# Kernel optimization log

Measured on AMD Instinct MI355X. Metric: run time of the kernel, lower is better.

The kernel has to match this reference:

```python
import jax, jax.numpy as jnp
import numpy as np

B, S, D, H, F = 2, 2048, 1024, 16, 64  # batch, seq, d_model, heads, head_dim


def setup_inputs() -> dict:
    key = jax.random.key(0)
    ks = jax.random.split(key, 7)
    return {
        "q": jax.random.normal(ks[0], (B, S, D), dtype=jnp.float32),
        "k": jax.random.normal(ks[1], (B, S, D), dtype=jnp.float32),
        "v": jax.random.normal(ks[2], (B, S, D), dtype=jnp.float32),
        "Wq": jax.random.normal(ks[3], (H, D, F), dtype=jnp.float32) * 0.02,
        "Wk": jax.random.normal(ks[4], (H, D, F), dtype=jnp.float32) * 0.02,
        "Wv": jax.random.normal(ks[5], (H, D, F), dtype=jnp.float32) * 0.02,
        "Wo": jax.random.normal(ks[6], (H * F, D), dtype=jnp.float32) * 0.02,
    }


def reference(q, k, v, Wq, Wk, Wv, Wo):
    head_dim = Wq.shape[-1]
    queries = jnp.einsum('bqo,hof->bhqf', q, Wq)
    keys = jnp.einsum('bko,hof->bhkf', k, Wk)
    values = jnp.einsum('bvo,hof->bhvf', v, Wv)
    # K.batch_dot(queries, keys, axes=[3,3]) -> [b,h,q,k]
    scores = jnp.einsum('bhqf,bhkf->bhqk', queries, keys) / jnp.sqrt(
        jnp.asarray(head_dim, dtype=queries.dtype))
    attn = jax.nn.softmax(scores, axis=-1)
    # Faithful to K.batch_dot(attn, values, axes=[2,2]):
    # contracts the QUERY axis of attn with the seq axis of values -> A^T V
    out4 = jnp.einsum('bhqk,bhqf->bhkf', attn, values)  # [b,h,s,f]
    b = out4.shape[0]
    # Faithful raw reshape [b,h,s,f] -> [b,s,h*f] (no transpose, as in original)
    out = out4.reshape(b, out4.shape[2], -1)
    return out @ Wo  # [b,s,d_model]
```

## Files before the change

kernel.cpp:

```cpp
#include <hip/hip_runtime.h>
#include <hip/hip_bf16.h>
#include <stdint.h>

#define Bc 2
#define Sc 2048
#define Dc 1024
#define Hc 16
#define Fc 64
constexpr int BHSF = Bc * Hc * Sc * Fc;

typedef __attribute__((ext_vector_type(8))) short bf16x8;
typedef __attribute__((ext_vector_type(4))) short bf16x4;
typedef __attribute__((ext_vector_type(4))) float f32x4;

#define MFMA16(a, b, c) __builtin_amdgcn_mfma_f32_16x16x32_bf16(a, b, c, 0, 0, 0)
#define EXP2(x) __builtin_amdgcn_exp2f(x)
#define SCALE2 0.18033688f

__device__ inline short f2bfn(float x) {
    __hip_bfloat16 h = __float2bfloat16(x);
    return __builtin_bit_cast(short, h);
}
__device__ inline uint32_t cvt2(float lo, float hi) {
    uint32_t a = (uint16_t)f2bfn(lo);
    uint32_t b = (uint16_t)f2bfn(hi);
    return a | (b << 16);
}
__device__ inline float bf2f(short s) {
    uint32_t u = ((uint32_t)(uint16_t)s) << 16;
    return __builtin_bit_cast(float, u);
}

__global__ __launch_bounds__(256) void tcvt_all_kernel(
    const float* __restrict__ Wq, const float* __restrict__ Wk,
    const float* __restrict__ Wv, const float* __restrict__ Wo,
    short* __restrict__ WqT, short* __restrict__ WkT,
    short* __restrict__ WvT, short* __restrict__ WoT)
{
    __shared__ short td[64 * 72];
    const int t = threadIdx.x;
    const int sr = t >> 2, sc = (t & 3) * 16;
    const int zp = blockIdx.z;
    const int m0 = blockIdx.x * 64;

    const float* in; short* out; int N, n0;
    if (zp < 48) {
        const int sel = zp >> 4, h = zp & 15;
        in  = ((sel == 0) ? Wq : (sel == 1) ? Wk : Wv) + (size_t)h * Dc * Fc;
        out = ((sel == 0) ? WqT : (sel == 1) ? WkT : WvT) + (size_t)h * Fc * Dc;
        N = Fc; n0 = 0;
    } else {
        in = Wo; out = WoT; N = Dc; n0 = (zp - 48) * 64;
    }

    const float* src = in + (size_t)(m0 + sr) * N + n0 + sc;
    #pragma unroll
    for (int i = 0; i < 16; i += 4) {
        f32x4 a = *(const f32x4*)(src + i);
        td[sr * 72 + sc + i + 0] = f2bfn(a[0]);
        td[sr * 72 + sc + i + 1] = f2bfn(a[1]);
        td[sr * 72 + sc + i + 2] = f2bfn(a[2]);
        td[sr * 72 + sc + i + 3] = f2bfn(a[3]);
    }
    __syncthreads();
    alignas(16) short vals[16];
    #pragma unroll
    for (int i = 0; i < 16; ++i) vals[i] = td[(sc + i) * 72 + sr];
    short* dst = out + (size_t)(n0 + sr) * Dc + m0 + sc;
    *(bf16x8*)dst       = *(const bf16x8*)&vals[0];
    *(bf16x8*)(dst + 8) = *(const bf16x8*)&vals[8];
}

__global__ __launch_bounds__(256) void proj_kernel(
    const float* __restrict__ xq, const float* __restrict__ xk,
    const float* __restrict__ xv,
    const short* __restrict__ WqT, const short* __restrict__ WkT,
    const short* __restrict__ WvT,
    short* __restrict__ Qo, short* __restrict__ Ko, short* __restrict__ VtO)
{
    const int mt = blockIdx.x, hp = blockIdx.y, z = blockIdx.z;
    const float* x  = (z == 0) ? xq : (z == 1) ? xk : xv;
    const short* Wt = ((z == 0) ? WqT : (z == 1) ? WkT : WvT) + (size_t)hp * 128 * Dc;
    const int m0 = mt * 128;

    __shared__ short xs[2][128 * 40];
    __shared__ short ws[2][128 * 40];

    const int t = threadIdx.x, lane = t & 63, w = t >> 6;
    const int wm = w >> 1, wn = w & 1;
    const int l15 = lane & 15, g = lane >> 4;
    const int str = t >> 1, stc = (t & 1) * 16;

    f32x4 xg[4]; bf16x8 wg[2];
    auto gload = [&](int d0) {
        const float* s = &x[(size_t)(m0 + str) * Dc + d0 + stc];
        #pragma unroll
        for (int j = 0; j < 4; ++j) xg[j] = ((const f32x4*)s)[j];
        const short* ww = &Wt[(size_t)str * Dc + d0 + stc];
        wg[0] = *(const bf16x8*)ww;
        wg[1] = *(const bf16x8*)(ww + 8);
    };
    auto swrite = [&](int buf) {
        bf16x8 p0, p1;
        #pragma unroll
        for (int i = 0; i < 4; ++i) {
            p0[i] = f2bfn(xg[0][i]); p0[4 + i] = f2bfn(xg[1][i]);
            p1[i] = f2bfn(xg[2][i]); p1[4 + i] = f2bfn(xg[3][i]);
        }
        *(bf16x8*)&xs[buf][str * 40 + stc]     = p0;
        *(bf16x8*)&xs[buf][str * 40 + stc + 8] = p1;
        *(bf16x8*)&ws[buf][str * 40 + stc]     = wg[0];
        *(bf16x8*)&ws[buf][str * 40 + stc + 8] = wg[1];
    };

    f32x4 acc[4][4];
    #pragma unroll
    for (int i = 0; i < 4; ++i)
        #pragma unroll
        for (int j = 0; j < 4; ++j) acc[i][j] = (f32x4){0.f, 0.f, 0.f, 0.f};

    gload(0); swrite(0); gload(32);

    auto step = [&](int d0, int cur) {
        __syncthreads();
        if (d0 + 32 < Dc) swrite(cur ^ 1);
        if (d0 + 64 < Dc) gload(d0 + 64);
        bf16x8 afr[4], bfr[4];
        #pragma unroll
        for (int ms = 0; ms < 4; ++ms)
            afr[ms] = *(const bf16x8*)&xs[cur][(wm * 64 + ms * 16 + l15) * 40 + g * 8];
        #pragma unroll
        for (int fb = 0; fb < 4; ++fb)
            bfr[fb] = *(const bf16x8*)&ws[cur][(wn * 64 + fb * 16 + l15) * 40 + g * 8];
        #pragma unroll
        for (int ms = 0; ms < 4; ++ms)
            #pragma unroll
            for (int fb = 0; fb < 4; ++fb)
                acc[ms][fb] = MFMA16(afr[ms], bfr[fb], acc[ms][fb]);
    };

    for (int d0 = 0; d0 < Dc; d0 += 64) {
        step(d0, 0);
        step(d0 + 32, 1);
    }

    const float oscale = (z == 0) ? SCALE2 : 1.0f;
    __syncthreads();
    {
        short* bb = wn ? &ws[0][0] : &xs[0][0];
        #pragma unroll
        for (int ms = 0; ms < 4; ++ms)
            #pragma unroll
            for (int fb = 0; fb < 4; ++fb)
                #pragma unroll
                for (int r = 0; r < 4; ++r)
                    bb[(wm * 64 + ms * 16 + g * 4 + r) * 80 + fb * 16 + l15] =
                        f2bfn(acc[ms][fb][r] * oscale);
    }
    __syncthreads();

    const int b = m0 >> 11, s0 = m0 & 2047;
    if (z < 2) {
        const int row = t & 127, half = t >> 7;
        const short* src = (half ? &ws[0][0] : &xs[0][0]) + row * 80;
        short* outp = ((z == 0) ? Qo : Ko)
                    + ((size_t)(b * Hc + hp * 2 + half) * Sc + s0 + row) * Fc;
        #pragma unroll
        for (int j = 0; j < 64; j += 8)
            *(bf16x8*)&outp[j] = *(const bf16x8*)&src[j];
    } else {
        const int fhr = t & 127, half = fhr >> 6, f = fhr & 63;
        const int colg = t >> 7;
        const short* src = half ? &ws[0][0] : &xs[0][0];
        short* o = VtO + ((size_t)(b * Hc + hp * 2 + half) * Fc + f) * Sc
                       + s0 + colg * 64;
        alignas(16) short vals[64];
        #pragma unroll
        for (int j = 0; j < 64; ++j) vals[j] = src[(colg * 64 + j) * 80 + f];
        #pragma unroll
        for (int j = 0; j < 64; j += 8)
            *(bf16x8*)(o + j) = *(const bf16x8*)&vals[j];
    }
}

__global__ __launch_bounds__(256) void stats_kernel(
    const short* __restrict__ Qg, const short* __restrict__ Kg,
    float* __restrict__ mrow)
{
    const int q0 = blockIdx.x * 128;
    const int bh = blockIdx.y;
    const short* Qb = Qg + (size_t)bh * Sc * Fc;
    const short* Kb = Kg + (size_t)bh * Sc * Fc;

    __shared__ short ksA[64 * 72], ksB[64 * 72];

    const int t = threadIdx.x, lane = t & 63, w = t >> 6;
    const int l15 = lane & 15, g = lane >> 4;
    const int sr4 = t >> 2, sc4 = (t & 3) * 16;

    bf16x8 qf[2][2];
    #pragma unroll
    for (int qs2 = 0; qs2 < 2; ++qs2)
        #pragma unroll
        for (int kc2 = 0; kc2 < 2; ++kc2)
            qf[qs2][kc2] = *(const bf16x8*)
                &Qb[(size_t)(q0 + w * 32 + qs2 * 16 + l15) * Fc + kc2 * 32 + g * 8];

    bf16x8 kr0, kr1;
    auto gload = [&](int kt) {
        const short* s = &Kb[(size_t)(kt + sr4) * Fc + sc4];
        kr0 = *(const bf16x8*)s;
        kr1 = *(const bf16x8*)(s + 8);
    };
    auto swrite = [&](short* d) {
        *(bf16x8*)&d[sr4 * 72 + sc4]     = kr0;
        *(bf16x8*)&d[sr4 * 72 + sc4 + 8] = kr1;
    };

    f32x4 ls[2];
    ls[0] = (f32x4){0.f, 0.f, 0.f, 0.f};
    ls[1] = (f32x4){0.f, 0.f, 0.f, 0.f};

    gload(0); swrite(ksA); gload(64);

    auto half = [&](int kt, const short* cur, short* nxt) {
        __syncthreads();
        if (kt + 64 < Sc) swrite(nxt);
        if (kt + 128 < Sc) gload(kt + 128);
        #pragma unroll
        for (int kf = 0; kf < 4; ++kf) {
            bf16x8 a0 = *(const bf16x8*)&cur[(kf * 16 + l15) * 72 + 0  + g * 8];
            bf16x8 a1 = *(const bf16x8*)&cur[(kf * 16 + l15) * 72 + 32 + g * 8];
            #pragma unroll
            for (int qs2 = 0; qs2 < 2; ++qs2) {
                f32x4 acc = (f32x4){0.f, 0.f, 0.f, 0.f};
                acc = MFMA16(a0, qf[qs2][0], acc);
                acc = MFMA16(a1, qf[qs2][1], acc);
                #pragma unroll
                for (int r = 0; r < 4; ++r) ls[qs2][r] += EXP2(acc[r]);
            }
        }
    };

    for (int kt = 0; kt < Sc; kt += 128) {
        half(kt,      ksA, ksB);
        half(kt + 64, ksB, ksA);
    }

    #pragma unroll
    for (int qs2 = 0; qs2 < 2; ++qs2) {
        float l = (ls[qs2][0] + ls[qs2][1]) + (ls[qs2][2] + ls[qs2][3]);
        l += __shfl_xor(l, 16, 64);
        l += __shfl_xor(l, 32, 64);
        if (lane < 16)
            mrow[bh * Sc + q0 + w * 32 + qs2 * 16 + l15] = __log2f(l);
    }
}

__global__ __launch_bounds__(256) void attn_kernel(
    const short* __restrict__ Qg, const short* __restrict__ Kg,
    const short* __restrict__ VtG, const float* __restrict__ mrow,
    short* __restrict__ O4a, short* __restrict__ O4b)
{
    const int k0 = blockIdx.x * 256;
    const int qh = blockIdx.y;
    const int bh = blockIdx.z;
    const int qbeg = qh * 1024, qend = qbeg + 1024;
    const short* Qb = Qg  + (size_t)bh * Sc * Fc;
    const short* Kb = Kg  + (size_t)bh * Sc * Fc;
    const short* Vb = VtG + (size_t)bh * Fc * Sc;
    const float* mb = mrow + (size_t)bh * Sc;

    __shared__ short qs[64 * 72];
    __shared__ short vt[64 * 72];
    __shared__ short pl[256 * 72];

    const int t = threadIdx.x, lane = t & 63, w = t >> 6;
    const int l15 = lane & 15, g = lane >> 4;
    const int sr8 = t >> 2, sc8 = (t & 3) * 16;

    bf16x8 kf[4][2];
    #pragma unroll
    for (int ks = 0; ks < 4; ++ks)
        #pragma unroll
        for (int kc = 0; kc < 2; ++kc)
            kf[ks][kc] = *(const bf16x8*)
                &Kb[(size_t)(k0 + w * 64 + ks * 16 + l15) * Fc + kc * 32 + g * 8];

    f32x4 oacc[4][4];
    #pragma unroll
    for (int i = 0; i < 4; ++i)
        #pragma unroll
        for (int j = 0; j < 4; ++j) oacc[i][j] = (f32x4){0.f, 0.f, 0.f, 0.f};

    bf16x8 qr0, qr1, vr0, vr1;
    auto gload = [&](int qn) {
        const short* s = &Qb[(size_t)(qn + sr8) * Fc + sc8];
        qr0 = *(const bf16x8*)s;
        qr1 = *(const bf16x8*)(s + 8);
        const short* v = &Vb[(size_t)sr8 * Sc + qn + sc8];
        vr0 = *(const bf16x8*)v;
        vr1 = *(const bf16x8*)(v + 8);
    };

    gload(qbeg);

    for (int q0 = qbeg; q0 < qend; q0 += 64) {
        __syncthreads();
        *(bf16x8*)&qs[sr8 * 72 + sc8]     = qr0;
        *(bf16x8*)&qs[sr8 * 72 + sc8 + 8] = qr1;
        *(bf16x8*)&vt[sr8 * 72 + sc8]     = vr0;
        *(bf16x8*)&vt[sr8 * 72 + sc8 + 8] = vr1;
        if (q0 + 64 < qend) gload(q0 + 64);
        f32x4 mq[4];
        #pragma unroll
        for (int qf = 0; qf < 4; ++qf)
            mq[qf] = *(const f32x4*)&mb[q0 + qf * 16 + g * 4];
        __syncthreads();

        #pragma unroll
        for (int qf = 0; qf < 4; ++qf) {
            bf16x8 qa0 = *(const bf16x8*)&qs[(qf * 16 + l15) * 72 + 0  + g * 8];
            bf16x8 qa1 = *(const bf16x8*)&qs[(qf * 16 + l15) * 72 + 32 + g * 8];
            #pragma unroll
            for (int ks = 0; ks < 4; ++ks) {
                f32x4 acc = (f32x4){0.f, 0.f, 0.f, 0.f};
                acc = MFMA16(qa0, kf[ks][0], acc);
                acc = MFMA16(qa1, kf[ks][1], acc);
                uint2 pv;
                pv.x = cvt2(EXP2(acc[0] - mq[qf][0]), EXP2(acc[1] - mq[qf][1]));
                pv.y = cvt2(EXP2(acc[2] - mq[qf][2]), EXP2(acc[3] - mq[qf][3]));
                *(uint2*)&pl[(w * 64 + ks * 16 + l15) * 72 + qf * 16 + g * 4] = pv;
            }
        }
        __syncthreads();

        #pragma unroll
        for (int qc = 0; qc < 64; qc += 32) {
            bf16x8 pa[4], vbf[4];
            #pragma unroll
            for (int ks = 0; ks < 4; ++ks)
                pa[ks] = *(const bf16x8*)&pl[(w * 64 + ks * 16 + l15) * 72 + qc + g * 8];
            #pragma unroll
            for (int fb = 0; fb < 4; ++fb)
                vbf[fb] = *(const bf16x8*)&vt[(fb * 16 + l15) * 72 + qc + g * 8];
            #pragma unroll
            for (int ks = 0; ks < 4; ++ks)
                #pragma unroll
                for (int fb = 0; fb < 4; ++fb)
                    oacc[ks][fb] = MFMA16(pa[ks], vbf[fb], oacc[ks][fb]);
        }
    }

    __syncthreads();
    #pragma unroll
    for (int ks = 0; ks < 4; ++ks)
        #pragma unroll
        for (int fb = 0; fb < 4; ++fb)
            #pragma unroll
            for (int r = 0; r < 4; ++r)
                pl[(w * 64 + ks * 16 + g * 4 + r) * 72 + fb * 16 + l15] =
                    f2bfn(oacc[ks][fb][r]);
    __syncthreads();
    {
        short* O = qh ? O4b : O4a;
        short* o = O + ((size_t)bh * Sc + k0 + t) * Fc;
        #pragma unroll
        for (int j = 0; j < 64; j += 8)
            *(bf16x8*)&o[j] = *(const bf16x8*)&pl[t * 72 + j];
    }
}

__global__ __launch_bounds__(256) void outgemm_kernel(
    const short* __restrict__ Aa, const short* __restrict__ Ab,
    const short* __restrict__ WoT, float* __restrict__ out)
{
    const int m0 = blockIdx.x * 128, n0 = blockIdx.y * 64;

    __shared__ short asA[128 * 72], asB[128 * 72];
    __shared__ short wsA[64 * 72],  wsB[64 * 72];

    const int t = threadIdx.x, lane = t & 63, w = t >> 6;
    const int l15 = lane & 15, g = lane >> 4;
    const int ar = t >> 1, ac = (t & 1) * 32;
    const int wr = t >> 2, wc = (t & 3) * 16;

    bf16x8 ag0[4], ag1[4], wg[2];
    auto gload = [&](int d0) {
        const short* s0 = &Aa[(size_t)(m0 + ar) * Dc + d0 + ac];
        const short* s1 = &Ab[(size_t)(m0 + ar) * Dc + d0 + ac];
        #pragma unroll
        for (int j = 0; j < 4; ++j) { ag0[j] = *(const bf16x8*)(s0 + 8 * j);
                                      ag1[j] = *(const bf16x8*)(s1 + 8 * j); }
        const short* ww = &WoT[(size_t)(n0 + wr) * Dc + d0 + wc];
        wg[0] = *(const bf16x8*)ww;
        wg[1] = *(const bf16x8*)(ww + 8);
    };
    auto swrite = [&](short* asD, short* wsD) {
        #pragma unroll
        for (int j = 0; j < 4; ++j) {
            bf16x8 r;
            #pragma unroll
            for (int i = 0; i < 8; ++i)
                r[i] = f2bfn(bf2f(ag0[j][i]) + bf2f(ag1[j][i]));
            *(bf16x8*)&asD[ar * 72 + ac + 8 * j] = r;
        }
        *(bf16x8*)&wsD[wr * 72 + wc]     = wg[0];
        *(bf16x8*)&wsD[wr * 72 + wc + 8] = wg[1];
    };

    f32x4 acc[2][4];
    #pragma unroll
    for (int i = 0; i < 2; ++i)
        #pragma unroll
        for (int j = 0; j < 4; ++j) acc[i][j] = (f32x4){0.f, 0.f, 0.f, 0.f};

    gload(0); swrite(asA, wsA); gload(64);

    auto half = [&](int d0, const short* asC, const short* wsC,
                    short* asN, short* wsN) {
        __syncthreads();
        if (d0 + 64 < Dc) swrite(asN, wsN);
        if (d0 + 128 < Dc) gload(d0 + 128);
        #pragma unroll
        for (int kc = 0; kc < 64; kc += 32) {
            bf16x8 afr[2], bfr[4];
            #pragma unroll
            for (int ms = 0; ms < 2; ++ms)
                afr[ms] = *(const bf16x8*)&asC[(w * 32 + ms * 16 + l15) * 72 + kc + g * 8];
            #pragma unroll
            for (int nb = 0; nb < 4; ++nb)
                bfr[nb] = *(const bf16x8*)&wsC[(nb * 16 + l15) * 72 + kc + g * 8];
            #pragma unroll
            for (int ms = 0; ms < 2; ++ms)
                #pragma unroll
                for (int nb = 0; nb < 4; ++nb)
                    acc[ms][nb] = MFMA16(afr[ms], bfr[nb], acc[ms][nb]);
        }
    };

    for (int d0 = 0; d0 < Dc; d0 += 128) {
        half(d0,      asA, wsA, asB, wsB);
        half(d0 + 64, asB, wsB, asA, wsA);
    }

    #pragma unroll
    for (int ms = 0; ms < 2; ++ms)
        #pragma unroll
        for (int nb = 0; nb < 4; ++nb)
            #pragma unroll
            for (int r = 0; r < 4; ++r)
                out[(size_t)(m0 + w * 32 + ms * 16 + g * 4 + r) * 1024
                    + n0 + nb * 16 + l15] = acc[ms][nb][r];
}

extern "C" void kernel_launch(void* const* d_in, const int* in_sizes, int n_in,
                              void* d_out, int out_size, void* d_ws, size_t ws_size,
                              hipStream_t stream) {
    (void)in_sizes; (void)n_in; (void)out_size; (void)ws_size;
    const float* q  = (const float*)d_in[0];
    const float* k  = (const float*)d_in[1];
    const float* v  = (const float*)d_in[2];
    const float* Wq = (const float*)d_in[3];
    const float* Wk = (const float*)d_in[4];
    const float* Wv = (const float*)d_in[5];
    const float* Wo = (const float*)d_in[6];
    float* out = (float*)d_out;

    short* Qw  = (short*)d_ws;
    short* Kw  = Qw  + BHSF;
    short* Vt  = Kw  + BHSF;
    short* O4a = Vt  + BHSF;
    short* O4b = O4a + BHSF;
    short* WqT = O4b + BHSF;
    short* WkT = WqT + Hc * Dc * Fc;
    short* WvT = WkT + Hc * Dc * Fc;
    short* WoT = WvT + Hc * Dc * Fc;
    float* mw  = (float*)(WoT + Dc * Dc);

    tcvt_all_kernel<<<dim3(16, 1, 64), 256, 0, stream>>>(Wq, Wk, Wv, Wo,
                                                         WqT, WkT, WvT, WoT);
    proj_kernel<<<dim3(32, 8, 3), 256, 0, stream>>>(q, k, v, WqT, WkT, WvT,
                                                    Qw, Kw, Vt);
    stats_kernel<<<dim3(16, 32), 256, 0, stream>>>(Qw, Kw, mw);
    attn_kernel<<<dim3(8, 2, 32), 256, 0, stream>>>(Qw, Kw, Vt, mw, O4a, O4b);
    outgemm_kernel<<<dim3(32, 16), 256, 0, stream>>>(O4a, O4b, WoT, out);
}
```

Measured before the change: 160.6 us.

## Load MFMA operands directly from global memory, dropping LDS staging and barriers

Across all four kernels, operand tiles that were staged through shared memory are now read straight from global memory into MFMA fragment registers. This applies to the weight tiles in the projection and output GEMMs, to K in the stats kernel, and to Q and V in the attention kernel. The attention kernel gives each wave its own private P buffer, which removes the per-iteration block barriers. The aim is to cut LDS traffic, LDS footprint and __syncthreads overhead so occupancy can rise, and launch bounds now request 3 blocks per CU. The trade-off is that global loads are no longer coalesced tiles, so more cache traffic and exposed global latency may result, plus higher register pressure from prefetched fragments.

```diff
diff --git a/kernel.cpp b/kernel.cpp
--- a/kernel.cpp
+++ b/kernel.cpp
@@ -10,7 +10,6 @@
 constexpr int BHSF = Bc * Hc * Sc * Fc;
 
 typedef __attribute__((ext_vector_type(8))) short bf16x8;
-typedef __attribute__((ext_vector_type(4))) short bf16x4;
 typedef __attribute__((ext_vector_type(4))) float f32x4;
 
 #define MFMA16(a, b, c) __builtin_amdgcn_mfma_f32_16x16x32_bf16(a, b, c, 0, 0, 0)
@@ -71,7 +70,7 @@
     *(bf16x8*)(dst + 8) = *(const bf16x8*)&vals[8];
 }
 
-__global__ __launch_bounds__(256) void proj_kernel(
+__global__ __launch_bounds__(256, 3) void proj_kernel(
     const float* __restrict__ xq, const float* __restrict__ xk,
     const float* __restrict__ xv,
     const short* __restrict__ WqT, const short* __restrict__ WkT,
@@ -84,23 +83,23 @@
     const int m0 = mt * 128;
 
     __shared__ short xs[2][128 * 40];
-    __shared__ short ws[2][128 * 40];
+    __shared__ short ob[128 * 72];
 
     const int t = threadIdx.x, lane = t & 63, w = t >> 6;
     const int wm = w >> 1, wn = w & 1;
     const int l15 = lane & 15, g = lane >> 4;
     const int str = t >> 1, stc = (t & 1) * 16;
 
-    f32x4 xg[4]; bf16x8 wg[2];
-    auto gload = [&](int d0) {
+    const short* wbase = Wt + (size_t)(wn * 64 + l15) * Dc + g * 8;
+
+    f32x4 xg[4];
+    bf16x8 wf[4], wfN[4];
+    auto gloadX = [&](int d0) {
         const float* s = &x[(size_t)(m0 + str) * Dc + d0 + stc];
         #pragma unroll
         for (int j = 0; j < 4; ++j) xg[j] = ((const f32x4*)s)[j];
-        const short* ww = &Wt[(size_t)str * Dc + d0 + stc];
-        wg[0] = *(const bf16x8*)ww;
-        wg[1] = *(const bf16x8*)(ww + 8);
-    };
-    auto swrite = [&](int buf) {
+    };
+    auto swriteX = [&](int buf) {
         bf16x8 p0, p1;
         #pragma unroll
         for (int i = 0; i < 4; ++i) {
@@ -109,8 +108,11 @@
         }
         *(bf16x8*)&xs[buf][str * 40 + stc]     = p0;
         *(bf16x8*)&xs[buf][str * 40 + stc + 8] = p1;
-        *(bf16x8*)&ws[buf][str * 40 + stc]     = wg[0];
-        *(bf16x8*)&ws[buf][str * 40 + stc + 8] = wg[1];
+    };
+    auto loadW = [&](int d0, bf16x8* dst) {
+        #pragma unroll
+        for (int fb = 0; fb < 4; ++fb)
+            dst[fb] = *(const bf16x8*)(wbase + (size_t)fb * 16 * Dc + d0);
     };
 
     f32x4 acc[4][4];
@@ -119,67 +121,61 @@
         #pragma unroll
         for (int j = 0; j < 4; ++j) acc[i][j] = (f32x4){0.f, 0.f, 0.f, 0.f};
 
-    gload(0); swrite(0); gload(32);
-
-    auto step = [&](int d0, int cur) {
+    gloadX(0); swriteX(0); gloadX(32); loadW(0, wf);
+
+    for (int d0 = 0; d0 < Dc; d0 += 32) {
+        const int cur = (d0 >> 5) & 1;
         __syncthreads();
-        if (d0 + 32 < Dc) swrite(cur ^ 1);
-        if (d0 + 64 < Dc) gload(d0 + 64);
-        bf16x8 afr[4], bfr[4];
+        if (d0 + 32 < Dc) swriteX(cur ^ 1);
+        if (d0 + 64 < Dc) gloadX(d0 + 64);
+        if (d0 + 32 < Dc) loadW(d0 + 32, wfN);
+        bf16x8 afr[4];
         #pragma unroll
         for (int ms = 0; ms < 4; ++ms)
             afr[ms] = *(const bf16x8*)&xs[cur][(wm * 64 + ms * 16 + l15) * 40 + g * 8];
         #pragma unroll
-        for (int fb = 0; fb < 4; ++fb)
-            bfr[fb] = *(const bf16x8*)&ws[cur][(wn * 64 + fb * 16 + l15) * 40 + g * 8];
-        #pragma unroll
         for (int ms = 0; ms < 4; ++ms)
             #pragma unroll
             for (int fb = 0; fb < 4; ++fb)
-                acc[ms][fb] = MFMA16(afr[ms], bfr[fb], acc[ms][fb]);
-    };
-
-    for (int d0 = 0; d0 < Dc; d0 += 64) {
-        step(d0, 0);
-        step(d0 + 32, 1);
+                acc[ms][fb] = MFMA16(afr[ms], wf[fb], acc[ms][fb]);
+        #pragma unroll
+        for (int fb = 0; fb < 4; ++fb) wf[fb] = wfN[fb];
     }
 
     const float oscale = (z == 0) ? SCALE2 : 1.0f;
-    __syncthreads();
-    {
-        short* bb = wn ? &ws[0][0] : &xs[0][0];
-        #pragma unroll
-        for (int ms = 0; ms < 4; ++ms)
-            #pragma unroll
-            for (int fb = 0; fb < 4; ++fb)
+    const int b = m0 >> 11, s0 = m0 & 2047;
+    #pragma unroll
+    for (int p = 0; p < 2; ++p) {
+        __syncthreads();
+        if (wn == p) {
+            #pragma unroll
+            for (int ms = 0; ms < 4; ++ms)
                 #pragma unroll
-                for (int r = 0; r < 4; ++r)
-                    bb[(wm * 64 + ms * 16 + g * 4 + r) * 80 + fb * 16 + l15] =
-                        f2bfn(acc[ms][fb][r] * oscale);
-    }
-    __syncthreads();
-
-    const int b = m0 >> 11, s0 = m0 & 2047;
-    if (z < 2) {
-        const int row = t & 127, half = t >> 7;
-        const short* src = (half ? &ws[0][0] : &xs[0][0]) + row * 80;
-        short* outp = ((z == 0) ? Qo : Ko)
-                    + ((size_t)(b * Hc + hp * 2 + half) * Sc + s0 + row) * Fc;
-        #pragma unroll
-        for (int j = 0; j < 64; j += 8)
-            *(bf16x8*)&outp[j] = *(const bf16x8*)&src[j];
-    } else {
-        const int fhr = t & 127, half = fhr >> 6, f = fhr & 63;
-        const int colg = t >> 7;
-        const short* src = half ? &ws[0][0] : &xs[0][0];
-        short* o = VtO + ((size_t)(b * Hc + hp * 2 + half) * Fc + f) * Sc
-                       + s0 + colg * 64;
-        alignas(16) short vals[64];
-        #pragma unroll
-        for (int j = 0; j < 64; ++j) vals[j] = src[(colg * 64 + j) * 80 + f];
-        #pragma unroll
-        for (int j = 0; j < 64; j += 8)
-            *(bf16x8*)(o + j) = *(const bf16x8*)&vals[j];
+                for (int fb = 0; fb < 4; ++fb)
+                    #pragma unroll
+                    for (int r = 0; r < 4; ++r)
+                        ob[(wm * 64 + ms * 16 + g * 4 + r) * 72 + fb * 16 + l15] =
+                            f2bfn(acc[ms][fb][r] * oscale);
+        }
+        __syncthreads();
+        const int h = hp * 2 + p;
+        if (z < 2) {
+            const int row = t >> 1, c0 = (t & 1) * 32;
+            short* outp = ((z == 0) ? Qo : Ko)
+                        + ((size_t)(b * Hc + h) * Sc + s0 + row) * Fc + c0;
+            #pragma unroll
+            for (int j = 0; j < 32; j += 8)
+                *(bf16x8*)&outp[j] = *(const bf16x8*)&ob[row * 72 + c0 + j];
+        } else {
+            const int f = t >> 2, cg = (t & 3) * 32;
+            short* o = VtO + ((size_t)(b * Hc + h) * Fc + f) * Sc + s0 + cg;
+            alignas(16) short vals[32];
+            #pragma unroll
+            for (int j = 0; j < 32; ++j) vals[j] = ob[(cg + j) * 72 + f];
+            #pragma unroll
+            for (int j = 0; j < 32; j += 8)
+                *(bf16x8*)(o + j) = *(const bf16x8*)&vals[j];
+        }
     }
 }
 
@@ -192,11 +188,8 @@
     const short* Qb = Qg + (size_t)bh * Sc * Fc;
     const short* Kb = Kg + (size_t)bh * Sc * Fc;
 
-    __shared__ short ksA[64 * 72], ksB[64 * 72];
-
     const int t = threadIdx.x, lane = t & 63, w = t >> 6;
     const int l15 = lane & 15, g = lane >> 4;
-    const int sr4 = t >> 2, sc4 = (t & 3) * 16;
 
     bf16x8 qf[2][2];
     #pragma unroll
@@ -206,45 +199,24 @@
             qf[qs2][kc2] = *(const bf16x8*)
                 &Qb[(size_t)(q0 + w * 32 + qs2 * 16 + l15) * Fc + kc2 * 32 + g * 8];
 
-    bf16x8 kr0, kr1;
-    auto gload = [&](int kt) {
-        const short* s = &Kb[(size_t)(kt + sr4) * Fc + sc4];
-        kr0 = *(const bf16x8*)s;
-        kr1 = *(const bf16x8*)(s + 8);
-    };
-    auto swrite = [&](short* d) {
-        *(bf16x8*)&d[sr4 * 72 + sc4]     = kr0;
-        *(bf16x8*)&d[sr4 * 72 + sc4 + 8] = kr1;
-    };
+    const short* kb = Kb + (size_t)l15 * Fc + g * 8;
 
     f32x4 ls[2];
     ls[0] = (f32x4){0.f, 0.f, 0.f, 0.f};
     ls[1] = (f32x4){0.f, 0.f, 0.f, 0.f};
 
-    gload(0); swrite(ksA); gload(64);
-
-    auto half = [&](int kt, const short* cur, short* nxt) {
-        __syncthreads();
-        if (kt + 64 < Sc) swrite(nxt);
-        if (kt + 128 < Sc) gload(kt + 128);
-        #pragma unroll
-        for (int kf = 0; kf < 4; ++kf) {
-            bf16x8 a0 = *(const bf16x8*)&cur[(kf * 16 + l15) * 72 + 0  + g * 8];
-            bf16x8 a1 = *(const bf16x8*)&cur[(kf * 16 + l15) * 72 + 32 + g * 8];
-            #pragma unroll
-            for (int qs2 = 0; qs2 < 2; ++qs2) {
-                f32x4 acc = (f32x4){0.f, 0.f, 0.f, 0.f};
-                acc = MFMA16(a0, qf[qs2][0], acc);
-                acc = MFMA16(a1, qf[qs2][1], acc);
-                #pragma unroll
-                for (int r = 0; r < 4; ++r) ls[qs2][r] += EXP2(acc[r]);
-            }
-        }
-    };
-
-    for (int kt = 0; kt < Sc; kt += 128) {
-        half(kt,      ksA, ksB);
-        half(kt + 64, ksB, ksA);
+    #pragma unroll 4
+    for (int kr = 0; kr < Sc; kr += 16) {
+        bf16x8 a0 = *(const bf16x8*)(kb + (size_t)kr * Fc);
+        bf16x8 a1 = *(const bf16x8*)(kb + (size_t)kr * Fc + 32);
+        #pragma unroll
+        for (int qs2 = 0; qs2 < 2; ++qs2) {
+            f32x4 acc = (f32x4){0.f, 0.f, 0.f, 0.f};
+            acc = MFMA16(a0, qf[qs2][0], acc);
+            acc = MFMA16(a1, qf[qs2][1], acc);
+            #pragma unroll
+            for (int r = 0; r < 4; ++r) ls[qs2][r] += EXP2(acc[r]);
+        }
     }
 
     #pragma unroll
@@ -257,7 +229,7 @@
     }
 }
 
-__global__ __launch_bounds__(256) void attn_kernel(
+__global__ __launch_bounds__(256, 3) void attn_kernel(
     const short* __restrict__ Qg, const short* __restrict__ Kg,
     const short* __restrict__ VtG, const float* __restrict__ mrow,
     short* __restrict__ O4a, short* __restrict__ O4b)
@@ -271,13 +243,11 @@
     const short* Vb = VtG + (size_t)bh * Fc * Sc;
     const float* mb = mrow + (size_t)bh * Sc;
 
-    __shared__ short qs[64 * 72];
-    __shared__ short vt[64 * 72];
-    __shared__ short pl[256 * 72];
+    __shared__ short pl[4][64 * 72];
 
     const int t = threadIdx.x, lane = t & 63, w = t >> 6;
     const int l15 = lane & 15, g = lane >> 4;
-    const int sr8 = t >> 2, sc8 = (t & 3) * 16;
+    short* plw = &pl[w][0];
 
     bf16x8 kf[4][2];
     #pragma unroll
@@ -287,63 +257,42 @@
             kf[ks][kc] = *(const bf16x8*)
                 &Kb[(size_t)(k0 + w * 64 + ks * 16 + l15) * Fc + kc * 32 + g * 8];
 
+    const short* qbase = Qb + (size_t)l15 * Fc + g * 8;
+    const short* vbase = Vb + (size_t)l15 * Sc + g * 8;
+
     f32x4 oacc[4][4];
     #pragma unroll
     for (int i = 0; i < 4; ++i)
         #pragma unroll
         for (int j = 0; j < 4; ++j) oacc[i][j] = (f32x4){0.f, 0.f, 0.f, 0.f};
 
-    bf16x8 qr0, qr1, vr0, vr1;
-    auto gload = [&](int qn) {
-        const short* s = &Qb[(size_t)(qn + sr8) * Fc + sc8];
-        qr0 = *(const bf16x8*)s;
-        qr1 = *(const bf16x8*)(s + 8);
-        const short* v = &Vb[(size_t)sr8 * Sc + qn + sc8];
-        vr0 = *(const bf16x8*)v;
-        vr1 = *(const bf16x8*)(v + 8);
-    };
-
-    gload(qbeg);
-
     for (int q0 = qbeg; q0 < qend; q0 += 64) {
-        __syncthreads();
-        *(bf16x8*)&qs[sr8 * 72 + sc8]     = qr0;
-        *(bf16x8*)&qs[sr8 * 72 + sc8 + 8] = qr1;
-        *(bf16x8*)&vt[sr8 * 72 + sc8]     = vr0;
-        *(bf16x8*)&vt[sr8 * 72 + sc8 + 8] = vr1;
-        if (q0 + 64 < qend) gload(q0 + 64);
-        f32x4 mq[4];
-        #pragma unroll
-        for (int qf = 0; qf < 4; ++qf)
-            mq[qf] = *(const f32x4*)&mb[q0 + qf * 16 + g * 4];
-        __syncthreads();
-
         #pragma unroll
         for (int qf = 0; qf < 4; ++qf) {
-            bf16x8 qa0 = *(const bf16x8*)&qs[(qf * 16 + l15) * 72 + 0  + g * 8];
-            bf16x8 qa1 = *(const bf16x8*)&qs[(qf * 16 + l15) * 72 + 32 + g * 8];
+            const int q = q0 + qf * 16;
+            bf16x8 qa0 = *(const bf16x8*)(qbase + (size_t)q * Fc);
+            bf16x8 qa1 = *(const bf16x8*)(qbase + (size_t)q * Fc + 32);
+            f32x4 mq = *(const f32x4*)&mb[q + g * 4];
             #pragma unroll
             for (int ks = 0; ks < 4; ++ks) {
                 f32x4 acc = (f32x4){0.f, 0.f, 0.f, 0.f};
                 acc = MFMA16(qa0, kf[ks][0], acc);
                 acc = MFMA16(qa1, kf[ks][1], acc);
                 uint2 pv;
-                pv.x = cvt2(EXP2(acc[0] - mq[qf][0]), EXP2(acc[1] - mq[qf][1]));
-                pv.y = cvt2(EXP2(acc[2] - mq[qf][2]), EXP2(acc[3] - mq[qf][3]));
-                *(uint2*)&pl[(w * 64 + ks * 16 + l15) * 72 + qf * 16 + g * 4] = pv;
+                pv.x = cvt2(EXP2(acc[0] - mq[0]), EXP2(acc[1] - mq[1]));
+                pv.y = cvt2(EXP2(acc[2] - mq[2]), EXP2(acc[3] - mq[3]));
+                *(uint2*)&plw[(ks * 16 + l15) * 72 + qf * 16 + g * 4] = pv;
             }
         }
-        __syncthreads();
-
         #pragma unroll
         for (int qc = 0; qc < 64; qc += 32) {
             bf16x8 pa[4], vbf[4];
             #pragma unroll
             for (int ks = 0; ks < 4; ++ks)
-                pa[ks] = *(const bf16x8*)&pl[(w * 64 + ks * 16 + l15) * 72 + qc + g * 8];
+                pa[ks] = *(const bf16x8*)&plw[(ks * 16 + l15) * 72 + qc + g * 8];
             #pragma unroll
             for (int fb = 0; fb < 4; ++fb)
-                vbf[fb] = *(const bf16x8*)&vt[(fb * 16 + l15) * 72 + qc + g * 8];
+                vbf[fb] = *(const bf16x8*)(vbase + (size_t)fb * 16 * Sc + q0 + qc);
             #pragma unroll
             for (int ks = 0; ks < 4; ++ks)
                 #pragma unroll
@@ -352,61 +301,64 @@
         }
     }
 
-    __syncthreads();
     #pragma unroll
     for (int ks = 0; ks < 4; ++ks)
         #pragma unroll
         for (int fb = 0; fb < 4; ++fb)
             #pragma unroll
             for (int r = 0; r < 4; ++r)
-                pl[(w * 64 + ks * 16 + g * 4 + r) * 72 + fb * 16 + l15] =
+                plw[(ks * 16 + g * 4 + r) * 72 + fb * 16 + l15] =
                     f2bfn(oacc[ks][fb][r]);
     __syncthreads();
     {
+        const short* plf = &pl[0][0];
         short* O = qh ? O4b : O4a;
         short* o = O + ((size_t)bh * Sc + k0 + t) * Fc;
         #pragma unroll
         for (int j = 0; j < 64; j += 8)
-            *(bf16x8*)&o[j] = *(const bf16x8*)&pl[t * 72 + j];
-    }
-}
-
-__global__ __launch_bounds__(256) void outgemm_kernel(
+            *(bf16x8*)&o[j] = *(const bf16x8*)&plf[t * 72 + j];
+    }
+}
+
+__global__ __launch_bounds__(256, 3) void outgemm_kernel(
     const short* __restrict__ Aa, const short* __restrict__ Ab,
     const short* __restrict__ WoT, float* __restrict__ out)
 {
     const int m0 = blockIdx.x * 128, n0 = blockIdx.y * 64;
 
-    __shared__ short asA[128 * 72], asB[128 * 72];
-    __shared__ short wsA[64 * 72],  wsB[64 * 72];
+    __shared__ short as_[2][128 * 72];
 
     const int t = threadIdx.x, lane = t & 63, w = t >> 6;
     const int l15 = lane & 15, g = lane >> 4;
     const int ar = t >> 1, ac = (t & 1) * 32;
-    const int wr = t >> 2, wc = (t & 3) * 16;
-
-    bf16x8 ag0[4], ag1[4], wg[2];
-    auto gload = [&](int d0) {
+
+    const short* wbase = WoT + (size_t)(n0 + l15) * Dc + g * 8;
+
+    bf16x8 ag0[4], ag1[4], wf[8], wfN[8];
+    auto gloadA = [&](int d0) {
         const short* s0 = &Aa[(size_t)(m0 + ar) * Dc + d0 + ac];
         const short* s1 = &Ab[(size_t)(m0 + ar) * Dc + d0 + ac];
         #pragma unroll
         for (int j = 0; j < 4; ++j) { ag0[j] = *(const bf16x8*)(s0 + 8 * j);
                                       ag1[j] = *(const bf16x8*)(s1 + 8 * j); }
-        const short* ww = &WoT[(size_t)(n0 + wr) * Dc + d0 + wc];
-        wg[0] = *(const bf16x8*)ww;
-        wg[1] = *(const bf16x8*)(ww + 8);
-    };
-    auto swrite = [&](short* asD, short* wsD) {
+    };
+    auto swriteA = [&](int buf) {
         #pragma unroll
         for (int j = 0; j < 4; ++j) {
             bf16x8 r;
             #pragma unroll
             for (int i = 0; i < 8; ++i)
                 r[i] = f2bfn(bf2f(ag0[j][i]) + bf2f(ag1[j][i]));
-            *(bf16x8*)&asD[ar * 72 + ac + 8 * j] = r;
-        }
-        *(bf16x8*)&wsD[wr * 72 + wc]     = wg[0];
-        *(bf16x8*)&wsD[wr * 72 + wc + 8] = wg[1];
+            *(bf16x8*)&as_[buf][ar * 72 + ac + 8 * j] = r;
+        }
+    };
+    auto loadW = [&](int d0, bf16x8* dst) {
+        #pragma unroll
+        for (int nb = 0; nb < 4; ++nb)
+            #pragma unroll
+            for (int kc = 0; kc < 2; ++kc)
+                dst[nb * 2 + kc] = *(const bf16x8*)
+                    (wbase + (size_t)nb * 16 * Dc + d0 + kc * 32);
     };
 
     f32x4 acc[2][4];
@@ -415,33 +367,29 @@
         #pragma unroll
         for (int j = 0; j < 4; ++j) acc[i][j] = (f32x4){0.f, 0.f, 0.f, 0.f};
 
-    gload(0); swrite(asA, wsA); gload(64);
-
-    auto half = [&](int d0, const short* asC, const short* wsC,
-                    short* asN, short* wsN) {
+    gloadA(0); swriteA(0); gloadA(64); loadW(0, wf);
+
+    for (int d0 = 0; d0 < Dc; d0 += 64) {
+        const int cur = (d0 >> 6) & 1;
         __syncthreads();
-        if (d0 + 64 < Dc) swrite(asN, wsN);
-        if (d0 + 128 < Dc) gload(d0 + 128);
-        #pragma unroll
-        for (int kc = 0; kc < 64; kc += 32) {
-            bf16x8 afr[2], bfr[4];
+        if (d0 + 64 < Dc)  swriteA(cur ^ 1);
+        if (d0 + 128 < Dc) gloadA(d0 + 128);
+        if (d0 + 64 < Dc)  loadW(d0 + 64, wfN);
+        #pragma unroll
+        for (int kc = 0; kc < 2; ++kc) {
+            bf16x8 afr[2];
             #pragma unroll
             for (int ms = 0; ms < 2; ++ms)
-                afr[ms] = *(const bf16x8*)&asC[(w * 32 + ms * 16 + l15) * 72 + kc + g * 8];
-            #pragma unroll
-            for (int nb = 0; nb < 4; ++nb)
-                bfr[nb] = *(const bf16x8*)&wsC[(nb * 16 + l15) * 72 + kc + g * 8];
+                afr[ms] = *(const bf16x8*)
+                    &as_[cur][(w * 32 + ms * 16 + l15) * 72 + kc * 32 + g * 8];
             #pragma unroll
             for (int ms = 0; ms < 2; ++ms)
                 #pragma unroll
                 for (int nb = 0; nb < 4; ++nb)
-                    acc[ms][nb] = MFMA16(afr[ms], bfr[nb], acc[ms][nb]);
-        }
-    };
-
-    for (int d0 = 0; d0 < Dc; d0 += 128) {
-        half(d0,      asA, wsA, asB, wsB);
-        half(d0 + 64, asB, wsB, asA, wsA);
+                    acc[ms][nb] = MFMA16(afr[ms], wf[nb * 2 + kc], acc[ms][nb]);
+        }
+        #pragma unroll
+        for (int i = 0; i < 8; ++i) wf[i] = wfN[i];
     }
 
     #pragma unroll
```

Result: slower. 272.9 us (+70.0%).

## Pre-convert activations to bf16 and stream projection tiles via LDS DMA

Applied to the files above, without the earlier changes.

Adds a separate kernel that converts the fp32 q/k/v activations to bf16 once, then rewrites the projection GEMM to load bf16 tiles straight into shared memory with global_load_lds, removing the per-block fp32 loads, register staging and conversion. The epilogue is split into two passes over a smaller shared buffer, and workspace buffers are aliased so the output staging reuses the converted-activation area. The proj kernel now reads half the activation bytes, but q/k/v are converted only once, whereas before each was converted by all 8 head-pair blocks. The cost is an extra launch and an extra round trip of the bf16 activations through memory, and the LDS tiles are unpadded (row stride 32), which may cause bank conflicts on fragment reads.

```diff
diff --git a/kernel.cpp b/kernel.cpp
--- a/kernel.cpp
+++ b/kernel.cpp
@@ -10,7 +10,6 @@
 constexpr int BHSF = Bc * Hc * Sc * Fc;
 
 typedef __attribute__((ext_vector_type(8))) short bf16x8;
-typedef __attribute__((ext_vector_type(4))) short bf16x4;
 typedef __attribute__((ext_vector_type(4))) float f32x4;
 
 #define MFMA16(a, b, c) __builtin_amdgcn_mfma_f32_16x16x32_bf16(a, b, c, 0, 0, 0)
@@ -29,6 +28,33 @@
 __device__ inline float bf2f(short s) {
     uint32_t u = ((uint32_t)(uint16_t)s) << 16;
     return __builtin_bit_cast(float, u);
+}
+
+__device__ inline void dma16(const short* g, short* l) {
+    __builtin_amdgcn_global_load_lds(
+        (const __attribute__((address_space(1))) void*)g,
+        (__attribute__((address_space(3))) void*)(uintptr_t)(uint32_t)(uintptr_t)l,
+        16, 0, 0);
+}
+
+__global__ __launch_bounds__(256) void xcvt_kernel(
+    const float* __restrict__ a, const float* __restrict__ b,
+    const float* __restrict__ c, short* __restrict__ out)
+{
+    const float* src = (blockIdx.y == 0) ? a : (blockIdx.y == 1) ? b : c;
+    const size_t base = (size_t)blockIdx.x * 4096 + threadIdx.x * 16;
+    const float* s = src + base;
+    short* d = out + (size_t)blockIdx.y * 4096 * 1024 + base;
+    f32x4 v0 = ((const f32x4*)s)[0], v1 = ((const f32x4*)s)[1];
+    f32x4 v2 = ((const f32x4*)s)[2], v3 = ((const f32x4*)s)[3];
+    bf16x8 p0, p1;
+    #pragma unroll
+    for (int i = 0; i < 4; ++i) {
+        p0[i] = f2bfn(v0[i]); p0[4 + i] = f2bfn(v1[i]);
+        p1[i] = f2bfn(v2[i]); p1[4 + i] = f2bfn(v3[i]);
+    }
+    *(bf16x8*)d       = p0;
+    *(bf16x8*)(d + 8) = p1;
 }
 
 __global__ __launch_bounds__(256) void tcvt_all_kernel(
@@ -72,45 +98,32 @@
 }
 
 __global__ __launch_bounds__(256) void proj_kernel(
-    const float* __restrict__ xq, const float* __restrict__ xk,
-    const float* __restrict__ xv,
+    const short* __restrict__ Xb,
     const short* __restrict__ WqT, const short* __restrict__ WkT,
     const short* __restrict__ WvT,
     short* __restrict__ Qo, short* __restrict__ Ko, short* __restrict__ VtO)
 {
     const int mt = blockIdx.x, hp = blockIdx.y, z = blockIdx.z;
-    const float* x  = (z == 0) ? xq : (z == 1) ? xk : xv;
+    const short* X  = Xb + (size_t)z * 4096 * Dc;
     const short* Wt = ((z == 0) ? WqT : (z == 1) ? WkT : WvT) + (size_t)hp * 128 * Dc;
     const int m0 = mt * 128;
 
-    __shared__ short xs[2][128 * 40];
-    __shared__ short ws[2][128 * 40];
+    __shared__ short sm[2][8192];
 
     const int t = threadIdx.x, lane = t & 63, w = t >> 6;
     const int wm = w >> 1, wn = w & 1;
     const int l15 = lane & 15, g = lane >> 4;
-    const int str = t >> 1, stc = (t & 1) * 16;
-
-    f32x4 xg[4]; bf16x8 wg[2];
-    auto gload = [&](int d0) {
-        const float* s = &x[(size_t)(m0 + str) * Dc + d0 + stc];
-        #pragma unroll
-        for (int j = 0; j < 4; ++j) xg[j] = ((const f32x4*)s)[j];
-        const short* ww = &Wt[(size_t)str * Dc + d0 + stc];
-        wg[0] = *(const bf16x8*)ww;
-        wg[1] = *(const bf16x8*)(ww + 8);
-    };
-    auto swrite = [&](int buf) {
-        bf16x8 p0, p1;
-        #pragma unroll
-        for (int i = 0; i < 4; ++i) {
-            p0[i] = f2bfn(xg[0][i]); p0[4 + i] = f2bfn(xg[1][i]);
-            p1[i] = f2bfn(xg[2][i]); p1[4 + i] = f2bfn(xg[3][i]);
-        }
-        *(bf16x8*)&xs[buf][str * 40 + stc]     = p0;
-        *(bf16x8*)&xs[buf][str * 40 + stc + 8] = p1;
-        *(bf16x8*)&ws[buf][str * 40 + stc]     = wg[0];
-        *(bf16x8*)&ws[buf][str * 40 + stc + 8] = wg[1];
+    const int lr = lane >> 2, lc = (lane & 3) * 8;
+
+    auto issue = [&](int buf, int d0) {
+        #pragma unroll
+        for (int i = 0; i < 2; ++i) {
+            const int rr = (w * 2 + i) * 16 + lr;
+            dma16(&X [(size_t)(m0 + rr) * Dc + d0 + lc],
+                  &sm[buf][(w * 2 + i) * 512]);
+            dma16(&Wt[(size_t)rr        * Dc + d0 + lc],
+                  &sm[buf][4096 + (w * 2 + i) * 512]);
+        }
     };
 
     f32x4 acc[4][4];
@@ -119,67 +132,63 @@
         #pragma unroll
         for (int j = 0; j < 4; ++j) acc[i][j] = (f32x4){0.f, 0.f, 0.f, 0.f};
 
-    gload(0); swrite(0); gload(32);
-
-    auto step = [&](int d0, int cur) {
-        __syncthreads();
-        if (d0 + 32 < Dc) swrite(cur ^ 1);
-        if (d0 + 64 < Dc) gload(d0 + 64);
+    issue(0, 0);
+
+    for (int d0 = 0; d0 < Dc; d0 += 32) {
+        const int cur = (d0 >> 5) & 1;
+        __syncthreads();
+        if (d0 + 32 < Dc) issue(cur ^ 1, d0 + 32);
+        const short* xb = &sm[cur][0];
+        const short* wb = &sm[cur][4096];
         bf16x8 afr[4], bfr[4];
         #pragma unroll
         for (int ms = 0; ms < 4; ++ms)
-            afr[ms] = *(const bf16x8*)&xs[cur][(wm * 64 + ms * 16 + l15) * 40 + g * 8];
+            afr[ms] = *(const bf16x8*)&xb[(wm * 64 + ms * 16 + l15) * 32 + g * 8];
         #pragma unroll
         for (int fb = 0; fb < 4; ++fb)
-            bfr[fb] = *(const bf16x8*)&ws[cur][(wn * 64 + fb * 16 + l15) * 40 + g * 8];
+            bfr[fb] = *(const bf16x8*)&wb[(wn * 64 + fb * 16 + l15) * 32 + g * 8];
         #pragma unroll
         for (int ms = 0; ms < 4; ++ms)
             #pragma unroll
             for (int fb = 0; fb < 4; ++fb)
                 acc[ms][fb] = MFMA16(afr[ms], bfr[fb], acc[ms][fb]);
-    };
-
-    for (int d0 = 0; d0 < Dc; d0 += 64) {
-        step(d0, 0);
-        step(d0 + 32, 1);
-    }
-
+    }
+
+    short* ob = &sm[0][0];
     const float oscale = (z == 0) ? SCALE2 : 1.0f;
-    __syncthreads();
-    {
-        short* bb = wn ? &ws[0][0] : &xs[0][0];
-        #pragma unroll
-        for (int ms = 0; ms < 4; ++ms)
-            #pragma unroll
-            for (int fb = 0; fb < 4; ++fb)
+    const int b = m0 >> 11, s0 = m0 & 2047;
+    #pragma unroll
+    for (int p = 0; p < 2; ++p) {
+        __syncthreads();
+        if (wn == p) {
+            #pragma unroll
+            for (int ms = 0; ms < 4; ++ms)
                 #pragma unroll
-                for (int r = 0; r < 4; ++r)
-                    bb[(wm * 64 + ms * 16 + g * 4 + r) * 80 + fb * 16 + l15] =
-                        f2bfn(acc[ms][fb][r] * oscale);
-    }
-    __syncthreads();
-
-    const int b = m0 >> 11, s0 = m0 & 2047;
-    if (z < 2) {
-        const int row = t & 127, half = t >> 7;
-        const short* src = (half ? &ws[0][0] : &xs[0][0]) + row * 80;
-        short* outp = ((z == 0) ? Qo : Ko)
-                    + ((size_t)(b * Hc + hp * 2 + half) * Sc + s0 + row) * Fc;
-        #pragma unroll
-        for (int j = 0; j < 64; j += 8)
-            *(bf16x8*)&outp[j] = *(const bf16x8*)&src[j];
-    } else {
-        const int fhr = t & 127, half = fhr >> 6, f = fhr & 63;
-        const int colg = t >> 7;
-        const short* src = half ? &ws[0][0] : &xs[0][0];
-        short* o = VtO + ((size_t)(b * Hc + hp * 2 + half) * Fc + f) * Sc
-                       + s0 + colg * 64;
-        alignas(16) short vals[64];
-        #pragma unroll
-        for (int j = 0; j < 64; ++j) vals[j] = src[(colg * 64 + j) * 80 + f];
-        #pragma unroll
-        for (int j = 0; j < 64; j += 8)
-            *(bf16x8*)(o + j) = *(const bf16x8*)&vals[j];
+                for (int fb = 0; fb < 4; ++fb)
+                    #pragma unroll
+                    for (int r = 0; r < 4; ++r)
+                        ob[(wm * 64 + ms * 16 + g * 4 + r) * 72 + fb * 16 + l15] =
+                            f2bfn(acc[ms][fb][r] * oscale);
+        }
+        __syncthreads();
+        const int h = hp * 2 + p;
+        if (z < 2) {
+            const int row = t >> 1, c0 = (t & 1) * 32;
+            short* outp = ((z == 0) ? Qo : Ko)
+                        + ((size_t)(b * Hc + h) * Sc + s0 + row) * Fc + c0;
+            #pragma unroll
+            for (int j = 0; j < 32; j += 8)
+                *(bf16x8*)&outp[j] = *(const bf16x8*)&ob[row * 72 + c0 + j];
+        } else {
+            const int f = t >> 2, cg = (t & 3) * 32;
+            short* o = VtO + ((size_t)(b * Hc + h) * Fc + f) * Sc + s0 + cg;
+            alignas(16) short vals[32];
+            #pragma unroll
+            for (int j = 0; j < 32; ++j) vals[j] = ob[(cg + j) * 72 + f];
+            #pragma unroll
+            for (int j = 0; j < 32; j += 8)
+                *(bf16x8*)(o + j) = *(const bf16x8*)&vals[j];
+        }
     }
 }
 
@@ -467,20 +476,22 @@
     const float* Wo = (const float*)d_in[6];
     float* out = (float*)d_out;
 
-    short* Qw  = (short*)d_ws;
+    short* Xb  = (short*)d_ws;
+    short* O4a = Xb;
+    short* O4b = Xb + BHSF;
+    short* Qw  = Xb  + (size_t)3 * 4096 * Dc;
     short* Kw  = Qw  + BHSF;
     short* Vt  = Kw  + BHSF;
-    short* O4a = Vt  + BHSF;
-    short* O4b = O4a + BHSF;
-    short* WqT = O4b + BHSF;
+    short* WqT = Vt  + BHSF;
     short* WkT = WqT + Hc * Dc * Fc;
     short* WvT = WkT + Hc * Dc * Fc;
     short* WoT = WvT + Hc * Dc * Fc;
     float* mw  = (float*)(WoT + Dc * Dc);
 
+    xcvt_kernel<<<dim3(1024, 3), 256, 0, stream>>>(q, k, v, Xb);
     tcvt_all_kernel<<<dim3(16, 1, 64), 256, 0, stream>>>(Wq, Wk, Wv, Wo,
                                                          WqT, WkT, WvT, WoT);
-    proj_kernel<<<dim3(32, 8, 3), 256, 0, stream>>>(q, k, v, WqT, WkT, WvT,
+    proj_kernel<<<dim3(32, 8, 3), 256, 0, stream>>>(Xb, WqT, WkT, WvT,
                                                     Qw, Kw, Vt);
     stats_kernel<<<dim3(16, 32), 256, 0, stream>>>(Qw, Kw, mw);
     attn_kernel<<<dim3(8, 2, 32), 256, 0, stream>>>(Qw, Kw, Vt, mw, O4a, O4b);
```

Result: slower. 169.1 us (+5.3%).
